# Kernel tuning notes

Measured on AMD Instinct MI355X. Metric: run time of the kernel, lower is better.

## Reference

```python
import jax, jax.numpy as jnp
import numpy as np

STRIDE = 8
PAD = 8
KSZ = 16


def setup_inputs() -> dict:
    key = jax.random.key(0)
    k1, k2, k3 = jax.random.split(key, 3)
    B, Cin, Cout, L = 16, 512, 1, 4000
    inp = jax.random.normal(k1, (B, Cin, L), dtype=jnp.float32)
    # t60 in [0.1, 0.5) so that round(t60*100)-10 lands in [0, 40]
    t60s = 0.1 + 0.39 * jax.random.uniform(k2, (B // 2,), dtype=jnp.float32)
    kernel_weight = jax.random.uniform(k3, (41, Cin, Cout, KSZ), dtype=jnp.float32)
    return {"input": inp, "t60s": t60s, "kernel_weight": kernel_weight}


def reference(input, t60s, kernel_weight):
    # per-sample kernel index: round(t60*100).int().repeat(2) - 10
    idx = jnp.tile(jnp.round(t60s * 100.0).astype(jnp.int32), 2) - 10  # (B,)
    w = kernel_weight[idx]                      # (B, Cin, Cout, K) gathered per sample
    # torch conv_transpose1d(x, W) == conv(x with lhs_dilation=stride,
    #                                      flip_k(W).swap(Cin,Cout), pad=K-1-p)
    w = jnp.flip(jnp.swapaxes(w, 1, 2), axis=-1)  # (B, Cout, Cin, K)
    pad = KSZ - 1 - PAD

    def per_sample(x, wk):  # x: (Cin, L), wk: (Cout, Cin, K)
        y = jax.lax.conv_general_dilated(
            x[None], wk,
            window_strides=(1,),
            padding=[(pad, pad)],
            lhs_dilation=(STRIDE,),
            dimension_numbers=("NCH", "OIH", "NCH"),
        )
        return y[0]  # (Cout, L_out), L_out = (L-1)*stride - 2*PAD + K

    return jax.vmap(per_sample)(input, w)  # (B, Cout, L_out)
```

## Files before the change

### kernel.cpp

```cpp
#include <hip/hip_runtime.h>

#define L_IN   4000
#define CIN    512
#define KSZ    16
#define LOUT   31992
#define NQ     3999
#define QPB    256
#define RST    1088

__global__ __launch_bounds__(1024, 4)
void dereverb_kernel(const float* __restrict__ x,
                     const float* __restrict__ t60s,
                     const float* __restrict__ kw,
                     float* __restrict__ out)
{
    __shared__ float lds[8 * RST];

    const int b    = blockIdx.y;
    const int q0   = blockIdx.x * QPB;
    const int tid  = threadIdx.x;
    const int lane = tid & 63;
    const int wave = tid >> 6;

    float t60 = t60s[b & 7];
    int kidx = (int)rintf(t60 * 100.0f) - 10;
    kidx = __builtin_amdgcn_readfirstlane(kidx);
    const float4* wsrc = (const float4*)(kw + (size_t)kidx * (CIN * KSZ));

    ((float4*)lds)[tid]        = wsrc[tid];
    ((float4*)lds)[tid + 1024] = wsrc[tid + 1024];
    __syncthreads();

    const int qb  = q0 + 4 * lane;
    const int qbl = qb < 3996 ? qb : 3996;
    const int qan = (qb + 4) < NQ ? (qb + 4) : NQ;

    const float* xr = x + ((size_t)b * CIN + wave * 32) * L_IN;
    const float* xp = xr + qbl;
    const float* xq = xr + qan;

    const float4* wl = (const float4*)(lds + wave * 32 * KSZ);

    float acc[4][8];
    #pragma unroll
    for (int qi = 0; qi < 4; ++qi)
        #pragma unroll
        for (int r = 0; r < 8; ++r) acc[qi][r] = 0.0f;

    #pragma unroll 4
    for (int ci = 0; ci < 32; ++ci) {
        float4 a  = *(const float4*)xp;
        float  an = *xq;
        xp += L_IN;
        xq += L_IN;

        float4 wv[4];
        wv[0] = wl[0];
        wv[1] = wl[1];
        wv[2] = wl[2];
        wv[3] = wl[3];
        wl += 4;
        const float* wf = (const float*)wv;

        const float x0v[4] = {a.x, a.y, a.z, a.w};
        const float x1v[4] = {a.y, a.z, a.w, an};
        #pragma unroll
        for (int qi = 0; qi < 4; ++qi)
            #pragma unroll
            for (int r = 0; r < 8; ++r) {
                acc[qi][r] = fmaf(x1v[qi], wf[r],     acc[qi][r]);
                acc[qi][r] = fmaf(x0v[qi], wf[r + 8], acc[qi][r]);
            }
    }

    #pragma unroll
    for (int qi = 0; qi < 4; ++qi)
        if (qb + qi > NQ - 1)
            #pragma unroll
            for (int r = 0; r < 8; ++r) acc[qi][r] = 0.0f;

    const size_t obase = (size_t)b * LOUT + (size_t)q0 * 8;
    #pragma unroll
    for (int p = 0; p < 2; ++p) {
        __syncthreads();
        if (wave >= 8) {
            float* rp = lds + (wave - 8) * RST + lane * 17;
            #pragma unroll
            for (int qih = 0; qih < 2; ++qih)
                #pragma unroll
                for (int r = 0; r < 8; ++r)
                    rp[qih * 8 + r] = acc[2 * p + qih][r];
        }
        __syncthreads();
        if (wave < 8) {
            float* rp = lds + wave * RST + lane * 17;
            #pragma unroll
            for (int qih = 0; qih < 2; ++qih)
                #pragma unroll
                for (int r = 0; r < 8; ++r)
                    rp[qih * 8 + r] += acc[2 * p + qih][r];
        }
        __syncthreads();
        int k = tid >> 4, j = tid & 15;
        int tl = 32 * k + 16 * p + j;
        if (q0 * 8 + tl < LOUT) {
            float s = 0.0f;
            #pragma unroll
            for (int w = 0; w < 8; ++w)
                s += lds[w * RST + k * 17 + j];
            out[obase + tl] = s;
        }
    }
}

extern "C" void kernel_launch(void* const* d_in, const int* in_sizes, int n_in,
                              void* d_out, int out_size, void* d_ws, size_t ws_size,
                              hipStream_t stream) {
    const float* x    = (const float*)d_in[0];
    const float* t60s = (const float*)d_in[1];
    const float* kw   = (const float*)d_in[2];
    float* out = (float*)d_out;

    dim3 grid((NQ + QPB - 1) / QPB, 16);
    dereverb_kernel<<<grid, 1024, 0, stream>>>(x, t60s, kw, out);
}
```

Measured before the change: 193.1 us.

## Split input channels across two blocks with atomic output accumulation and prefetching

```diff
diff --git a/kernel.cpp b/kernel.cpp
--- a/kernel.cpp
+++ b/kernel.cpp
@@ -6,18 +6,20 @@
 #define LOUT   31992
 #define NQ     3999
 #define QPB    256
+#define CPB    256
 #define RST    1088
 
-__global__ __launch_bounds__(1024, 4)
+__global__ __launch_bounds__(512, 4)
 void dereverb_kernel(const float* __restrict__ x,
                      const float* __restrict__ t60s,
                      const float* __restrict__ kw,
                      float* __restrict__ out)
 {
-    __shared__ float lds[8 * RST];
+    __shared__ float lds[4 * RST];
 
     const int b    = blockIdx.y;
     const int q0   = blockIdx.x * QPB;
+    const int cih  = blockIdx.z;
     const int tid  = threadIdx.x;
     const int lane = tid & 63;
     const int wave = tid >> 6;
@@ -25,20 +27,19 @@
     float t60 = t60s[b & 7];
     int kidx = (int)rintf(t60 * 100.0f) - 10;
     kidx = __builtin_amdgcn_readfirstlane(kidx);
-    const float4* wsrc = (const float4*)(kw + (size_t)kidx * (CIN * KSZ));
+    const float4* wsrc = (const float4*)(kw + ((size_t)kidx * CIN + cih * CPB) * KSZ);
 
-    ((float4*)lds)[tid]        = wsrc[tid];
-    ((float4*)lds)[tid + 1024] = wsrc[tid + 1024];
+    ((float4*)lds)[tid]       = wsrc[tid];
+    ((float4*)lds)[tid + 512] = wsrc[tid + 512];
     __syncthreads();
 
     const int qb  = q0 + 4 * lane;
     const int qbl = qb < 3996 ? qb : 3996;
     const int qan = (qb + 4) < NQ ? (qb + 4) : NQ;
 
-    const float* xr = x + ((size_t)b * CIN + wave * 32) * L_IN;
+    const float* xr = x + ((size_t)b * CIN + cih * CPB + wave * 32) * L_IN;
     const float* xp = xr + qbl;
     const float* xq = xr + qan;
-
     const float4* wl = (const float4*)(lds + wave * 32 * KSZ);
 
     float acc[4][8];
@@ -47,31 +48,45 @@
         #pragma unroll
         for (int r = 0; r < 8; ++r) acc[qi][r] = 0.0f;
 
-    #pragma unroll 4
-    for (int ci = 0; ci < 32; ++ci) {
-        float4 a  = *(const float4*)xp;
-        float  an = *xq;
-        xp += L_IN;
-        xq += L_IN;
+#define FMA_BODY(A, AN, W0, W1, W2, W3) do {                        \
+        const float xl[4] = {(A).x, (A).y, (A).z, (A).w};           \
+        const float xh[4] = {(A).y, (A).z, (A).w, (AN)};            \
+        const float wa[8] = {(W0).x,(W0).y,(W0).z,(W0).w,           \
+                             (W1).x,(W1).y,(W1).z,(W1).w};          \
+        const float wb[8] = {(W2).x,(W2).y,(W2).z,(W2).w,           \
+                             (W3).x,(W3).y,(W3).z,(W3).w};          \
+        _Pragma("unroll")                                           \
+        for (int qi = 0; qi < 4; ++qi)                              \
+            _Pragma("unroll")                                       \
+            for (int r = 0; r < 8; ++r) {                           \
+                acc[qi][r] = fmaf(xh[qi], wa[r], acc[qi][r]);       \
+                acc[qi][r] = fmaf(xl[qi], wb[r], acc[qi][r]);       \
+            }                                                       \
+    } while (0)
 
-        float4 wv[4];
-        wv[0] = wl[0];
-        wv[1] = wl[1];
-        wv[2] = wl[2];
-        wv[3] = wl[3];
-        wl += 4;
-        const float* wf = (const float*)wv;
+    float4 a0 = *(const float4*)xp;
+    float  n0 = *xq;
+    float4 a1 = *(const float4*)(xp + L_IN);
+    float  n1 = *(xq + L_IN);
+    float4 w0 = wl[0], w1 = wl[1], w2 = wl[2], w3 = wl[3];
 
-        const float x0v[4] = {a.x, a.y, a.z, a.w};
-        const float x1v[4] = {a.y, a.z, a.w, an};
-        #pragma unroll
-        for (int qi = 0; qi < 4; ++qi)
-            #pragma unroll
-            for (int r = 0; r < 8; ++r) {
-                acc[qi][r] = fmaf(x1v[qi], wf[r],     acc[qi][r]);
-                acc[qi][r] = fmaf(x0v[qi], wf[r + 8], acc[qi][r]);
-            }
+    #pragma unroll 2
+    for (int ci = 0; ci < 30; ++ci) {
+        float4 a2 = *(const float4*)(xp + 2 * L_IN);
+        float  n2 = *(xq + 2 * L_IN);
+        float4 u0 = wl[4], u1 = wl[5], u2 = wl[6], u3 = wl[7];
+        FMA_BODY(a0, n0, w0, w1, w2, w3);
+        a0 = a1; n0 = n1; a1 = a2; n1 = n2;
+        w0 = u0; w1 = u1; w2 = u2; w3 = u3;
+        xp += L_IN; xq += L_IN; wl += 4;
     }
+    {
+        float4 u0 = wl[4], u1 = wl[5], u2 = wl[6], u3 = wl[7];
+        FMA_BODY(a0, n0, w0, w1, w2, w3);
+        a0 = a1; n0 = n1;
+        w0 = u0; w1 = u1; w2 = u2; w3 = u3;
+    }
+    FMA_BODY(a0, n0, w0, w1, w2, w3);
 
     #pragma unroll
     for (int qi = 0; qi < 4; ++qi)
@@ -83,8 +98,8 @@
     #pragma unroll
     for (int p = 0; p < 2; ++p) {
         __syncthreads();
-        if (wave >= 8) {
-            float* rp = lds + (wave - 8) * RST + lane * 17;
+        if (wave >= 4) {
+            float* rp = lds + (wave - 4) * RST + lane * 17;
             #pragma unroll
             for (int qih = 0; qih < 2; ++qih)
                 #pragma unroll
@@ -92,7 +107,7 @@
                     rp[qih * 8 + r] = acc[2 * p + qih][r];
         }
         __syncthreads();
-        if (wave < 8) {
+        if (wave < 4) {
             float* rp = lds + wave * RST + lane * 17;
             #pragma unroll
             for (int qih = 0; qih < 2; ++qih)
@@ -101,16 +116,21 @@
                     rp[qih * 8 + r] += acc[2 * p + qih][r];
         }
         __syncthreads();
-        int k = tid >> 4, j = tid & 15;
-        int tl = 32 * k + 16 * p + j;
-        if (q0 * 8 + tl < LOUT) {
-            float s = 0.0f;
-            #pragma unroll
-            for (int w = 0; w < 8; ++w)
-                s += lds[w * RST + k * 17 + j];
-            out[obase + tl] = s;
+        const int k = tid >> 4, j = tid & 15;
+        #pragma unroll
+        for (int kk = 0; kk < 2; ++kk) {
+            const int kc = k + 32 * kk;
+            const int tl = 32 * kc + 16 * p + j;
+            if (q0 * 8 + tl < LOUT) {
+                float s = lds[0 * RST + kc * 17 + j]
+                        + lds[1 * RST + kc * 17 + j]
+                        + lds[2 * RST + kc * 17 + j]
+                        + lds[3 * RST + kc * 17 + j];
+                unsafeAtomicAdd(&out[obase + tl], s);
+            }
         }
     }
+#undef FMA_BODY
 }
 
 extern "C" void kernel_launch(void* const* d_in, const int* in_sizes, int n_in,
@@ -121,6 +141,8 @@
     const float* kw   = (const float*)d_in[2];
     float* out = (float*)d_out;
 
-    dim3 grid((NQ + QPB - 1) / QPB, 16);
-    dereverb_kernel<<<grid, 1024, 0, stream>>>(x, t60s, kw, out);
+    hipMemsetAsync(d_out, 0, out_size, stream);
+
+    dim3 grid((NQ + QPB - 1) / QPB, 16, 2);
+    dereverb_kernel<<<grid, 512, 0, stream>>>(x, t60s, kw, out);
 }
```

Result: no change. 195.7 us (+1.4%).

## Split channel reduction into streaming partial-sum kernel plus separate reduce kernel

Applied to the files above, without the earlier changes.

```diff
diff --git a/kernel.cpp b/kernel.cpp
--- a/kernel.cpp
+++ b/kernel.cpp
@@ -1,18 +1,129 @@
 #include <hip/hip_runtime.h>
 
-#define L_IN   4000
-#define CIN    512
-#define KSZ    16
-#define LOUT   31992
-#define NQ     3999
-#define QPB    256
-#define RST    1088
+#define L_IN     4000
+#define CIN      512
+#define KSZ      16
+#define LOUT     31992
+#define NQ       3999
+#define CCH      32
+#define LOUT_PAD 32768
+#define NCH      16
+#define WS_FLOATS ((size_t)NCH * 16 * LOUT_PAD)
 
 __global__ __launch_bounds__(1024, 4)
-void dereverb_kernel(const float* __restrict__ x,
+void dereverb_stream(const float* __restrict__ x,
                      const float* __restrict__ t60s,
                      const float* __restrict__ kw,
-                     float* __restrict__ out)
+                     float* __restrict__ ws)
+{
+    __shared__ float wlds[CCH * KSZ];
+
+    const int c0   = blockIdx.x * CCH;
+    const int b    = blockIdx.y;
+    const int tid  = threadIdx.x;
+    const int lane = tid & 63;
+    const int wave = tid >> 6;
+
+    float t60 = t60s[b & 7];
+    int kidx = (int)rintf(t60 * 100.0f) - 10;
+    kidx = __builtin_amdgcn_readfirstlane(kidx);
+
+    if (tid < 128)
+        ((float4*)wlds)[tid] =
+            ((const float4*)(kw + ((size_t)kidx * CIN + c0) * KSZ))[tid];
+    __syncthreads();
+
+    const int qb  = wave * 256 + 4 * lane;
+    const int qbl = qb < 3996 ? qb : 3996;
+    const int qan = (qb + 4) < NQ ? (qb + 4) : NQ;
+
+    const float* xrow = x + ((size_t)b * CIN + c0) * L_IN;
+    const float* xp = xrow + qbl;
+    const float* xq = xrow + qan;
+    const float4* wl = (const float4*)wlds;
+
+    float acc[4][8];
+    #pragma unroll
+    for (int qi = 0; qi < 4; ++qi)
+        #pragma unroll
+        for (int r = 0; r < 8; ++r) acc[qi][r] = 0.0f;
+
+#define FMA_BODY(A, AN, W0, W1, W2, W3) do {                        \
+        const float xl[4] = {(A).x, (A).y, (A).z, (A).w};           \
+        const float xh[4] = {(A).y, (A).z, (A).w, (AN)};            \
+        const float wa[8] = {(W0).x,(W0).y,(W0).z,(W0).w,           \
+                             (W1).x,(W1).y,(W1).z,(W1).w};          \
+        const float wb[8] = {(W2).x,(W2).y,(W2).z,(W2).w,           \
+                             (W3).x,(W3).y,(W3).z,(W3).w};          \
+        _Pragma("unroll")                                           \
+        for (int qi = 0; qi < 4; ++qi)                              \
+            _Pragma("unroll")                                       \
+            for (int r = 0; r < 8; ++r) {                           \
+                acc[qi][r] = fmaf(xh[qi], wa[r], acc[qi][r]);       \
+                acc[qi][r] = fmaf(xl[qi], wb[r], acc[qi][r]);       \
+            }                                                       \
+    } while (0)
+
+    float4 a0 = *(const float4*)xp;
+    float  n0 = *xq;
+    float4 a1 = *(const float4*)(xp + L_IN);
+    float  n1 = *(xq + L_IN);
+    float4 w0 = wl[0], w1 = wl[1], w2 = wl[2], w3 = wl[3];
+
+    #pragma unroll 2
+    for (int ci = 0; ci < 30; ++ci) {
+        float4 a2 = *(const float4*)(xp + 2 * L_IN);
+        float  n2 = *(xq + 2 * L_IN);
+        float4 u0 = wl[4], u1 = wl[5], u2 = wl[6], u3 = wl[7];
+        FMA_BODY(a0, n0, w0, w1, w2, w3);
+        a0 = a1; n0 = n1; a1 = a2; n1 = n2;
+        w0 = u0; w1 = u1; w2 = u2; w3 = u3;
+        xp += L_IN; xq += L_IN; wl += 4;
+    }
+    {
+        float4 u0 = wl[4], u1 = wl[5], u2 = wl[6], u3 = wl[7];
+        FMA_BODY(a0, n0, w0, w1, w2, w3);
+        a0 = a1; n0 = n1;
+        w0 = u0; w1 = u1; w2 = u2; w3 = u3;
+    }
+    FMA_BODY(a0, n0, w0, w1, w2, w3);
+
+    float* op = ws + (size_t)(blockIdx.x * 16 + b) * LOUT_PAD + (size_t)8 * qb;
+    #pragma unroll
+    for (int qi = 0; qi < 4; ++qi) {
+        float4 lo = {acc[qi][0], acc[qi][1], acc[qi][2], acc[qi][3]};
+        float4 hi = {acc[qi][4], acc[qi][5], acc[qi][6], acc[qi][7]};
+        ((float4*)(op + 8 * qi))[0] = lo;
+        ((float4*)(op + 8 * qi))[1] = hi;
+    }
+#undef FMA_BODY
+}
+
+__global__ __launch_bounds__(256, 8)
+void dereverb_reduce(const float* __restrict__ ws, float* __restrict__ out)
+{
+    const int b  = blockIdx.y;
+    const int t4 = blockIdx.x * 256 + threadIdx.x;
+    if (t4 >= LOUT / 4) return;
+
+    const float4* p = (const float4*)(ws + (size_t)b * LOUT_PAD) + t4;
+    float4 s = {0.0f, 0.0f, 0.0f, 0.0f};
+    #pragma unroll
+    for (int c = 0; c < NCH; ++c) {
+        float4 v = *p;
+        s.x += v.x; s.y += v.y; s.z += v.z; s.w += v.w;
+        p += (size_t)16 * LOUT_PAD / 4;
+    }
+    ((float4*)(out + (size_t)b * LOUT))[t4] = s;
+}
+
+#define QPB 256
+#define RST 1088
+__global__ __launch_bounds__(1024, 4)
+void dereverb_fallback(const float* __restrict__ x,
+                       const float* __restrict__ t60s,
+                       const float* __restrict__ kw,
+                       float* __restrict__ out)
 {
     __shared__ float lds[8 * RST];
 
@@ -38,7 +149,6 @@
     const float* xr = x + ((size_t)b * CIN + wave * 32) * L_IN;
     const float* xp = xr + qbl;
     const float* xq = xr + qan;
-
     const float4* wl = (const float4*)(lds + wave * 32 * KSZ);
 
     float acc[4][8];
@@ -55,10 +165,7 @@
         xq += L_IN;
 
         float4 wv[4];
-        wv[0] = wl[0];
-        wv[1] = wl[1];
-        wv[2] = wl[2];
-        wv[3] = wl[3];
+        wv[0] = wl[0]; wv[1] = wl[1]; wv[2] = wl[2]; wv[3] = wl[3];
         wl += 4;
         const float* wf = (const float*)wv;
 
@@ -121,6 +228,14 @@
     const float* kw   = (const float*)d_in[2];
     float* out = (float*)d_out;
 
-    dim3 grid((NQ + QPB - 1) / QPB, 16);
-    dereverb_kernel<<<grid, 1024, 0, stream>>>(x, t60s, kw, out);
-}
+    if (ws_size >= WS_FLOATS * sizeof(float) && d_ws != nullptr) {
+        float* ws = (float*)d_ws;
+        dim3 g1(CIN / CCH, 16);
+        dereverb_stream<<<g1, 1024, 0, stream>>>(x, t60s, kw, ws);
+        dim3 g2((LOUT / 4 + 255) / 256, 16);
+        dereverb_reduce<<<g2, 256, 0, stream>>>(ws, out);
+    } else {
+        dim3 grid((NQ + QPB - 1) / QPB, 16);
+        dereverb_fallback<<<grid, 1024, 0, stream>>>(x, t60s, kw, out);
+    }
+}
```

New measurement: 204.8 us. 1.06x slower.
